# Kernel optimization log

Hardware: AMD Instinct MI355X
Metric: run time of the kernel (lower is better)

Reference implementation:

```python
import jax, jax.numpy as jnp
from jax import lax
import numpy as np

H = 52; W = 52; N = 31; VIS = 256; LANG = 256; HID = 256


def _conv(x, w, b):
    # NCHW conv, SAME padding, stride 1
    return lax.conv_general_dilated(x, w, (1, 1), 'SAME',
                                    dimension_numbers=('NCHW', 'OIHW', 'NCHW')) + b[None, :, None, None]


def setup_inputs() -> dict:
    key = jax.random.key(0)
    ks = jax.random.split(key, 12)

    def kaiming(k, shape):
        fan_in = shape[1] * shape[2] * shape[3]
        return (jax.random.normal(k, shape) * np.sqrt(2.0 / fan_in)).astype(jnp.float32)

    # full binary tree: node c's parent is (c-1)//2; adj[parent, child] = 1; root = 0
    adj = np.zeros((N, N), np.int32)
    for c in range(1, N):
        adj[(c - 1) // 2, c] = 1

    return {
        'vis_feat': jax.random.normal(ks[0], (1, VIS, H, W), jnp.float32),
        'lang_feat': jax.random.normal(ks[1], (N, LANG), jnp.float32),
        'mconv_w': kaiming(ks[2], (HID, 2 * VIS + LANG, 1, 1)), 'mconv_b': jnp.zeros((HID,), jnp.float32),
        'reset_w': kaiming(ks[3], (HID, 2 * HID, 3, 3)), 'reset_b': jnp.zeros((HID,), jnp.float32),
        'update_w': kaiming(ks[4], (HID, 2 * HID, 3, 3)), 'update_b': jnp.zeros((HID,), jnp.float32),
        'output_w': kaiming(ks[5], (HID, 2 * HID, 3, 3)), 'output_b': jnp.zeros((HID,), jnp.float32),
        'theta_v_w': kaiming(ks[6], (128, HID, 1, 1)), 'theta_v_b': jnp.zeros((128,), jnp.float32),
        'theta_l_w': kaiming(ks[7], (128, LANG, 1, 1)), 'theta_l_b': jnp.zeros((128,), jnp.float32),
        'psi_w': kaiming(ks[8], (1, 128, 1, 1)), 'psi_b': jnp.zeros((1,), jnp.float32),
        'W_w': kaiming(ks[9], (HID, HID, 1, 1)), 'W_b': jnp.zeros((HID,), jnp.float32),
        'adj': jnp.asarray(adj),
    }


def reference(vis_feat, lang_feat, mconv_w, mconv_b, reset_w, reset_b, update_w, update_b,
              output_w, output_b, theta_v_w, theta_v_b, theta_l_w, theta_l_b,
              psi_w, psi_b, W_w, W_b, adj):
    adj_np = np.asarray(adj)
    children = [np.nonzero(adj_np[i] > 0)[0] for i in range(adj_np.shape[0])]
    root = int(np.nonzero(adj_np.sum(axis=0) == 0)[0][0])
    hid = reset_w.shape[0]
    Hh, Ww = vis_feat.shape[2], vis_feat.shape[3]

    def gru_cell(x, child_h):
        # x: [1,hid,H,W], child_h: [L,1,hid,H,W]
        L = child_h.shape[0]
        ch_sum = child_h.sum(axis=0)  # [1,hid,H,W]
        z = jax.nn.sigmoid(_conv(jnp.concatenate([x, ch_sum], axis=1), update_w, update_b))
        xr = jnp.broadcast_to(x[None], (L,) + x.shape)
        r_in = jnp.concatenate([xr, child_h], axis=2).reshape(L, 2 * hid, Hh, Ww)
        r = jax.nn.sigmoid(_conv(r_in, reset_w, reset_b))[:, None]  # [L,1,hid,H,W]
        reset_hidden = (r * child_h).sum(axis=0)
        ri = jnp.tanh(_conv(jnp.concatenate([x, reset_hidden], axis=1), output_w, output_b))
        return (1 - z) * ri + z * ch_sum

    def node(idx):
        kids = children[idx]
        if len(kids) == 0:
            child_atts = jnp.zeros((1, 1, Hh, Ww), vis_feat.dtype)
            child_h = jnp.zeros((1, 1, hid, Hh, Ww), vis_feat.dtype)
        else:
            fs, ats = zip(*[node(int(c)) for c in kids])
            child_h = jnp.stack(fs)                  # [L,1,hid,H,W]
            child_atts = jnp.concatenate(ats, 0)     # [L,1,H,W]
        att_in = 1 - child_atts.mean(axis=0, keepdims=True)  # [1,1,H,W]
        ctx = att_in * vis_feat                              # [1,VIS,H,W]
        lang_map = jnp.broadcast_to(lang_feat[idx][None, :, None, None],
                                    (1, lang_feat.shape[1], Hh, Ww))
        nf = _conv(jnp.concatenate([vis_feat, ctx, lang_map], axis=1), mconv_w, mconv_b)
        f = jax.nn.softplus(_conv(nf, theta_v_w, theta_v_b) + _conv(lang_map, theta_l_w, theta_l_b))
        att = jax.nn.sigmoid(_conv(f, psi_w, psi_b))  # [1,1,H,W]
        Wy = _conv(att * nf, W_w, W_b)
        h = gru_cell(Wy, child_h)
        return h, att

    return node(root)
```

## Files before the change

### kernel.cpp

```cpp
#include <hip/hip_runtime.h>
#include <hip/hip_bf16.h>

typedef __hip_bfloat16 bf16;
typedef short bf16x8 __attribute__((ext_vector_type(8)));
typedef float f32x16 __attribute__((ext_vector_type(16)));

static constexpr int  HW2 = 52;
static constexpr int  P2  = 2704;
static constexpr long CHW = 692224L;
static constexpr long PADE  = 884736L;
static constexpr long SLOT_W = 589824L;

static constexpr long O_HPB = 0;
static constexpr long O_XP  = O_HPB + 24*(PADE/2);
static constexpr long O_CS  = O_XP  + 16*(PADE/2);
static constexpr long O_RH  = O_CS  + 8*(PADE/2);
static constexpr long O_Z   = O_RH  + 8*(PADE/2);
static constexpr long O_RX  = O_Z   + 16*(CHW/2);
static constexpr long O_T1  = O_RX  + 8*(CHW/2);
static constexpr long O_T2  = O_T1  + 8*(CHW/2);
static constexpr long O_VPT = O_T2  + 8*(CHW/2);
static constexpr long O_ATT = O_VPT + (long)P2*768;
static constexpr long O_TVL = O_ATT + 31L*P2;
static constexpr long O_WL  = O_TVL + 31L*128;
static constexpr long O_S   = O_WL  + 31L*256;
static constexpr long O_WRE = O_S   + 768L*256;
static constexpr long WS_FLOATS = O_WRE + (3L*2*SLOT_W)/2;
static constexpr long ZERO_F4 = O_Z / 4;

struct ConvDesc {
  const bf16 *in0, *in1;
  const bf16 *w;
  void *out;
  const bf16 *zb;
  const bf16 *h1, *h2;
  long mode;
};
struct ConvBatch { ConvDesc d[32]; };

__device__ __forceinline__ float sigf(float x){ return 1.f/(1.f+expf(-x)); }
__device__ __forceinline__ float softplusf(float x){ return fmaxf(x,0.f) + log1pf(expf(-fabsf(x))); }
__device__ __forceinline__ long padidx(int px, int c){
  int y = px/HW2, x = px - y*HW2;
  return ((long)(c>>4)*3456 + (y+1)*64 + (x+1))*16 + (c&15);
}
__device__ __forceinline__ void gl_lds16(const bf16* g, bf16* l){
  __builtin_amdgcn_global_load_lds((const __attribute__((address_space(1))) void*)g,
                                   (__attribute__((address_space(3))) void*)l, 16, 0, 0);
}

__global__ __launch_bounds__(256) void k_zero(float4* __restrict__ dst, long n4)
{
  long e = (long)blockIdx.x*256 + threadIdx.x;
  if (e < n4) dst[e] = make_float4(0.f,0.f,0.f,0.f);
}

__global__ __launch_bounds__(256) void k_compose(
    const float* __restrict__ theta_v_w, const float* __restrict__ W_w,
    const float* __restrict__ mconv_w, float* __restrict__ S)
{
  int row = blockIdx.x, col = threadIdx.x;
  const float* A; int arow; int bcol;
  if      (row < 128) { A = theta_v_w; arow = row;     bcol = col;       }
  else if (row < 256) { A = theta_v_w; arow = row-128; bcol = col + 256; }
  else if (row < 512) { A = W_w;       arow = row-256; bcol = col;       }
  else                { A = W_w;       arow = row-512; bcol = col + 256; }
  float a = 0.f;
  for (int k=0;k<256;k++) a = fmaf(A[arow*256+k], mconv_w[k*768 + bcol], a);
  S[(long)row*256 + col] = a;
}

__global__ __launch_bounds__(256) void k_nodevec(
    const float* __restrict__ lang, const float* __restrict__ mconv_w, const float* __restrict__ mconv_b,
    const float* __restrict__ theta_v_w, const float* __restrict__ theta_v_b,
    const float* __restrict__ theta_l_w, const float* __restrict__ theta_l_b,
    const float* __restrict__ W_w, float* __restrict__ tvl, float* __restrict__ WLg)
{
  __shared__ float lf[256], lc[256];
  int n = blockIdx.x, tid = threadIdx.x;
  lf[tid] = lang[n*256 + tid];
  __syncthreads();
  float a = mconv_b[tid];
  for (int k=0;k<256;k++) a = fmaf(mconv_w[tid*768 + 512 + k], lf[k], a);
  lc[tid] = a;
  __syncthreads();
  if (tid < 128) {
    float b = theta_v_b[tid] + theta_l_b[tid];
    for (int k=0;k<256;k++) {
      b = fmaf(theta_v_w[tid*256+k], lc[k], b);
      b = fmaf(theta_l_w[tid*256+k], lf[k], b);
    }
    tvl[n*128 + tid] = b;
  }
  float c2 = 0.f;
  for (int k=0;k<256;k++) c2 = fmaf(W_w[tid*256+k], lc[k], c2);
  WLg[n*256 + tid] = c2;
}

__global__ __launch_bounds__(256) void k_vis_gemm(
    const float* __restrict__ S, const float* __restrict__ vis, float* __restrict__ VP)
{
  int p = blockIdx.x*256 + threadIdx.x; if (p >= P2) return;
  int m0 = blockIdx.y*4;
  float a0=0,a1=0,a2=0,a3=0;
  for (int k=0;k<256;k++) {
    float v = vis[k*P2 + p];
    a0 = fmaf(S[(m0+0)*256+k], v, a0);
    a1 = fmaf(S[(m0+1)*256+k], v, a1);
    a2 = fmaf(S[(m0+2)*256+k], v, a2);
    a3 = fmaf(S[(m0+3)*256+k], v, a3);
  }
  VP[(long)(m0+0)*P2+p]=a0; VP[(long)(m0+1)*P2+p]=a1;
  VP[(long)(m0+2)*P2+p]=a2; VP[(long)(m0+3)*P2+p]=a3;
}

__global__ __launch_bounds__(256) void k_vpt(const float* __restrict__ VP, float* __restrict__ VPT)
{
  __shared__ float t[64][65];
  int p0 = blockIdx.x*64, m0 = blockIdx.y*64;
  int c = threadIdx.x & 63, rb = threadIdx.x >> 6;
  for (int r = rb; r < 64; r += 4) {
    int p = p0 + c;
    t[r][c] = (p < P2) ? VP[(long)(m0 + r)*P2 + p] : 0.f;
  }
  __syncthreads();
  for (int r = rb; r < 64; r += 4) {
    int p = p0 + r;
    if (p < P2) VPT[(long)p*768 + (m0 + c)] = t[c][r];
  }
}

__global__ __launch_bounds__(256) void k_wre(
    const float* __restrict__ wu, const float* __restrict__ wr, const float* __restrict__ wo,
    bf16* __restrict__ dst)
{
  long e = (long)blockIdx.x*256 + threadIdx.x;
  int gate = blockIdx.y;
  const float* src = (gate==0) ? wu : (gate==1) ? wr : wo;
  int ci  = e & 15;       long t1 = e >> 4;
  int co  = t1 & 255;     long t2 = t1 >> 8;
  int tap = t2 % 9;       long t3 = t2 / 9;
  int cb  = t3 & 15;      int inp = (int)(t3 >> 4);
  int cin = inp*256 + cb*16 + ci;
  dst[(long)gate*2*SLOT_W + e] = __float2bfloat16(src[((long)co*512 + cin)*9 + tap]);
}

__global__ __launch_bounds__(256) void k_pre(
    const float* __restrict__ VPT, const float* __restrict__ tvl, const float* __restrict__ WLg,
    const float* __restrict__ psi_w, const float* __restrict__ psi_b, const float* __restrict__ W_b,
    float* __restrict__ attp, bf16* __restrict__ xpad, bf16* __restrict__ cspad,
    const bf16* __restrict__ hpb, int n0, int is_leaf)
{
  __shared__ float satt[16], sattin[16];
  const int tid = threadIdx.x, lane = tid & 63, wv = tid >> 6;
  const int i = blockIdx.y, n = n0 + i;
  const int pb = blockIdx.x*16;
  #pragma unroll
  for (int j=0;j<4;j++){
    int sl = wv*4 + j, p = pb + sl;
    float ai = 1.f;
    if (!is_leaf)
      ai = 1.f - 0.5f*(attp[(long)(2*n+1)*P2+p] + attp[(long)(2*n+2)*P2+p]);
    const float* vp = VPT + (long)p*768;
    float t0 = vp[lane]      + ai*vp[128+lane] + tvl[n*128+lane];
    float t1 = vp[64+lane]   + ai*vp[192+lane] + tvl[n*128+64+lane];
    float s = psi_w[lane]*softplusf(t0) + psi_w[64+lane]*softplusf(t1);
    for (int o=32;o;o>>=1) s += __shfl_xor(s,o);
    if (lane==0){
      float av = sigf(s + psi_b[0]);
      satt[sl]=av; sattin[sl]=ai; attp[(long)n*P2+p]=av;
    }
  }
  __syncthreads();
  const int c = tid;
  bf16* xp = xpad + (long)i*PADE;
  bf16* cp = cspad + (long)i*PADE;
  const bf16* h1 = hpb + (long)((2*n+1)%24)*PADE;
  const bf16* h2 = hpb + (long)((2*n+2)%24)*PADE;
  float wl = WLg[n*256+c], wb = W_b[c];
  for (int j=0;j<16;j++){
    int p = pb + j;
    long pi = padidx(p, c);
    const float* vp = VPT + (long)p*768;
    float wy = fmaf(satt[j], vp[256+c] + sattin[j]*vp[512+c] + wl, wb);
    xp[pi] = __float2bfloat16(wy);
    if (!is_leaf)
      cp[pi] = __float2bfloat16(__bfloat162float(h1[pi]) + __bfloat162float(h2[pi]));
  }
}

__global__ __launch_bounds__(256, 4) void k_conv(ConvBatch cb, int Z,
    const float* __restrict__ ub, const float* __restrict__ ob)
{
  __shared__ __align__(16) bf16 simg[8*64*16];
  __shared__ __align__(16) bf16 swt[9*64*16];
  const int L = blockIdx.x + 11*(blockIdx.y + 4*blockIdx.z);
  const int T = 44*Z;
  int V = L;
  if ((T & 7) == 0) V = (L & 7)*(T >> 3) + (L >> 3);
  const int dz  = V / 44;
  const int rr  = V - dz*44;
  const int coh = rr / 11;
  const int pxb = rr - coh*11;
  const ConvDesc d = cb.d[dz];
  const int pxbase = pxb * 256;
  const int co0    = coh * 64;
  const int tid = threadIdx.x, wv = tid >> 6, lane = tid & 63;
  const int wpx = wv * 64;
  const int y0 = pxbase / HW2;
  const int r0 = (y0 > 46) ? 46 : y0;
  const int khalf = lane >> 5;

  int apos[2];
  #pragma unroll
  for (int f=0; f<2; f++) {
    int p = pxbase + wpx + f*32 + (lane & 31);
    if (p >= P2) p = P2-1;
    int y = p / HW2, x = p - y*HW2;
    apos[f] = ((y - r0)*64 + x)*16 + khalf*8;
  }
  const int bpos = (lane & 31)*16 + khalf*8;

  f32x16 acc[2][2];
  #pragma unroll
  for (int f=0;f<2;f++)
    #pragma unroll
    for (int g=0;g<2;g++)
      #pragma unroll
      for (int r=0;r<16;r++) acc[f][g][r] = 0.f;

  const int ninp = d.in1 ? 2 : 1;
  for (int inp = 0; inp < ninp; ++inp) {
    const bf16* __restrict__ in = inp ? d.in1 : d.in0;
    const bf16* __restrict__ wg = d.w + (long)inp * SLOT_W;
    for (int c16 = 0; c16 < 16; ++c16) {
      __syncthreads();
      const long slab = (long)c16*55296 + (long)r0*1024;
      for (int i = wv; i < 34; i += 4) {
        if (i < 16)
          gl_lds16(in + slab + i*512 + lane*8, simg + i*512);
        else {
          int j = i - 16, tap = j >> 1, q = j & 1;
          gl_lds16(wg + (((long)c16*9 + tap)*256 + co0 + q*32)*16 + lane*8,
                   swt + tap*1024 + q*512);
        }
      }
      __syncthreads();
      #pragma unroll
      for (int tap = 0; tap < 9; ++tap) {
        const int toff = ((tap/3)*64 + (tap%3))*16;
        bf16x8 a0 = *(const bf16x8*)(simg + apos[0] + toff);
        bf16x8 a1 = *(const bf16x8*)(simg + apos[1] + toff);
        bf16x8 b0 = *(const bf16x8*)(swt + tap*1024 + bpos);
        bf16x8 b1 = *(const bf16x8*)(swt + tap*1024 + bpos + 512);
        acc[0][0] = __builtin_amdgcn_mfma_f32_32x32x16_bf16(a0, b0, acc[0][0], 0, 0, 0);
        acc[0][1] = __builtin_amdgcn_mfma_f32_32x32x16_bf16(a0, b1, acc[0][1], 0, 0, 0);
        acc[1][0] = __builtin_amdgcn_mfma_f32_32x32x16_bf16(a1, b0, acc[1][0], 0, 0, 0);
        acc[1][1] = __builtin_amdgcn_mfma_f32_32x32x16_bf16(a1, b1, acc[1][1], 0, 0, 0);
      }
    }
  }

  const int m = (int)d.mode;
  #pragma unroll
  for (int f=0;f<2;f++) {
    #pragma unroll
    for (int g=0;g<2;g++) {
      #pragma unroll
      for (int r=0;r<16;r++) {
        int px = pxbase + wpx + f*32 + (r&3) + 8*(r>>2) + 4*khalf;
        if (px >= P2) continue;
        int co = co0 + g*32 + (lane & 31);
        float v = acc[f][g][r];
        if (m == 0) {
          ((bf16*)d.out)[(long)px*256 + co] = __float2bfloat16(v);
        } else if (m == 1) {
          ((bf16*)d.out)[(long)px*256 + co] = __float2bfloat16(sigf(v + ub[co]));
        } else {
          float z = __bfloat162float(d.zb[(long)px*256 + co]);
          long pi = padidx(px, co);
          float cs = 0.f;
          if (d.h1) cs = __bfloat162float(d.h1[pi]) + __bfloat162float(d.h2[pi]);
          ((bf16*)d.out)[pi] = __float2bfloat16((1.f - z)*tanhf(v + ob[co]) + z*cs);
        }
      }
    }
  }
}

__global__ __launch_bounds__(256) void k_fin(
    const bf16* __restrict__ ubuf, const bf16* __restrict__ obuf,
    bf16* __restrict__ hpb, const float* __restrict__ update_b,
    const float* __restrict__ output_b, int n0)
{
  const int c = threadIdx.x, i = blockIdx.y, n = n0 + i;
  const bf16* u = ubuf + (long)i*CHW;
  const bf16* o = obuf + (long)i*CHW;
  bf16* h = hpb + (long)(n%24)*PADE;
  float ubv = update_b[c], obv = output_b[c];
  for (int j=0;j<16;j++){
    int p = blockIdx.x*16 + j;
    long e = (long)p*256 + c;
    float z = sigf(__bfloat162float(u[e]) + ubv);
    h[padidx(p, c)] = __float2bfloat16((1.f - z)*tanhf(__bfloat162float(o[e]) + obv));
  }
}

__global__ __launch_bounds__(256) void k_rh(
    const bf16* __restrict__ rxb, const bf16* __restrict__ t1b, const bf16* __restrict__ t2b,
    bf16* __restrict__ rhpad, const bf16* __restrict__ hpb,
    const float* __restrict__ reset_b, int n0)
{
  const int c = threadIdx.x, i = blockIdx.y, n = n0 + i;
  const bf16* rx = rxb + (long)i*CHW;
  const bf16* t1 = t1b + (long)i*CHW;
  const bf16* t2 = t2b + (long)i*CHW;
  bf16* rh = rhpad + (long)i*PADE;
  const bf16* h1 = hpb + (long)((2*n+1)%24)*PADE;
  const bf16* h2 = hpb + (long)((2*n+2)%24)*PADE;
  float rb = reset_b[c];
  for (int j=0;j<16;j++){
    int p = blockIdx.x*16 + j;
    long e = (long)p*256 + c, pi = padidx(p, c);
    float a = __bfloat162float(rx[e]);
    float r1 = sigf(a + __bfloat162float(t1[e]) + rb);
    float r2 = sigf(a + __bfloat162float(t2[e]) + rb);
    rh[pi] = __float2bfloat16(r1*__bfloat162float(h1[pi]) + r2*__bfloat162float(h2[pi]));
  }
}

__global__ __launch_bounds__(256) void k_outh(const bf16* __restrict__ h0, float* __restrict__ out)
{
  __shared__ float t[64][65];
  int p0 = blockIdx.x*64, c0 = blockIdx.y*64;
  int c = threadIdx.x & 63, rb = threadIdx.x >> 6;
  for (int r = rb; r < 64; r += 4) {
    int p = p0 + r;
    t[r][c] = (p < P2) ? __bfloat162float(h0[padidx(p, c0 + c)]) : 0.f;
  }
  __syncthreads();
  for (int r = rb; r < 64; r += 4) {
    int p = p0 + c;
    if (p < P2) out[(long)(c0 + r)*P2 + p] = t[c][r];
  }
}
__global__ __launch_bounds__(256) void k_outa(const float* __restrict__ att0, float* __restrict__ out)
{
  int p = blockIdx.x*256 + threadIdx.x;
  if (p < P2) out[CHW + p] = att0[p];
}

extern "C" void kernel_launch(void* const* d_in, const int* in_sizes, int n_in,
                              void* d_out, int out_size, void* d_ws, size_t ws_size,
                              hipStream_t stream)
{
  const float* vis       = (const float*)d_in[0];
  const float* lang      = (const float*)d_in[1];
  const float* mconv_w   = (const float*)d_in[2];
  const float* mconv_b   = (const float*)d_in[3];
  const float* reset_w   = (const float*)d_in[4];
  const float* reset_b   = (const float*)d_in[5];
  const float* update_w  = (const float*)d_in[6];
  const float* update_b  = (const float*)d_in[7];
  const float* output_w  = (const float*)d_in[8];
  const float* output_b  = (const float*)d_in[9];
  const float* theta_v_w = (const float*)d_in[10];
  const float* theta_v_b = (const float*)d_in[11];
  const float* theta_l_w = (const float*)d_in[12];
  const float* theta_l_b = (const float*)d_in[13];
  const float* psi_w     = (const float*)d_in[14];
  const float* psi_b     = (const float*)d_in[15];
  const float* W_w       = (const float*)d_in[16];
  const float* W_b       = (const float*)d_in[17];

  if (ws_size < (size_t)WS_FLOATS * sizeof(float)) return;
  float* ws   = (float*)d_ws;
  bf16*  hpb  = (bf16*)(ws + O_HPB);
  bf16*  xpad = (bf16*)(ws + O_XP);
  bf16*  cspad= (bf16*)(ws + O_CS);
  bf16*  rhpad= (bf16*)(ws + O_RH);
  bf16*  zbuf = (bf16*)(ws + O_Z);
  bf16*  rxb  = (bf16*)(ws + O_RX);
  bf16*  t1b  = (bf16*)(ws + O_T1);
  bf16*  t2b  = (bf16*)(ws + O_T2);
  float* VPT  = ws + O_VPT;
  float* attp = ws + O_ATT;
  float* tvl  = ws + O_TVL;
  float* WLg  = ws + O_WL;
  float* S    = ws + O_S;
  bf16*  wre  = (bf16*)(ws + O_WRE);
  bf16*  wre_u = wre;
  bf16*  wre_r = wre + 2*SLOT_W;
  bf16*  wre_o = wre + 4*SLOT_W;
  float* VP   = (float*)zbuf;

  auto hslot = [&](int n){ return hpb + (long)(n%24)*PADE; };
  auto xp    = [&](int i){ return xpad  + (long)i*PADE; };
  auto csp   = [&](int i){ return cspad + (long)i*PADE; };
  auto rhp   = [&](int i){ return rhpad + (long)i*PADE; };
  auto zbp   = [&](int i){ return zbuf + (long)i*CHW; };
  auto obp   = [&](int i){ return rxb + (long)i*CHW; };

  k_zero<<<(ZERO_F4 + 255)/256, 256, 0, stream>>>((float4*)ws, ZERO_F4);
  k_wre<<<dim3(4608,3), 256, 0, stream>>>(update_w, reset_w, output_w, wre);
  k_compose<<<768, 256, 0, stream>>>(theta_v_w, W_w, mconv_w, S);
  k_nodevec<<<31, 256, 0, stream>>>(lang, mconv_w, mconv_b, theta_v_w, theta_v_b,
                                    theta_l_w, theta_l_b, W_w, tvl, WLg);
  k_vis_gemm<<<dim3(11,192), 256, 0, stream>>>(S, vis, VP);
  k_vpt<<<dim3(43,12), 256, 0, stream>>>(VP, VPT);

  {
    const int n0 = 15, B = 16;
    k_pre<<<dim3(169,B), 256, 0, stream>>>(VPT, tvl, WLg, psi_w, psi_b, W_b,
                                           attp, xpad, cspad, hpb, n0, 1);
    ConvBatch ca{};
    for (int i=0;i<B;i++) {
      ca.d[i]   = { xp(i), nullptr, wre_u, (void*)zbp(i), nullptr, nullptr, nullptr, 0 };
      ca.d[B+i] = { xp(i), nullptr, wre_o, (void*)obp(i), nullptr, nullptr, nullptr, 0 };
    }
    k_conv<<<dim3(11,4,2*B), 256, 0, stream>>>(ca, 2*B, update_b, output_b);
    k_fin<<<dim3(169,B), 256, 0, stream>>>(zbuf, rxb, hpb, update_b, output_b, n0);
  }

  const int Ln0[4] = {7, 3, 1, 0};
  const int LnB[4] = {8, 4, 2, 1};
  for (int li=0; li<4; li++) {
    int n0 = Ln0[li]; int B = LnB[li];
    k_pre<<<dim3(169,B), 256, 0, stream>>>(VPT, tvl, WLg, psi_w, psi_b, W_b,
                                           attp, xpad, cspad, hpb, n0, 0);
    ConvBatch ca{};
    for (int i=0;i<B;i++) {
      int n = n0 + i;
      ca.d[4*i+0] = { xp(i), csp(i),    wre_u,          (void*)zbp(i),              nullptr, nullptr, nullptr, 1 };
      ca.d[4*i+1] = { xp(i), nullptr,   wre_r,          (void*)(rxb + (long)i*CHW), nullptr, nullptr, nullptr, 0 };
      ca.d[4*i+2] = { hslot(2*n+1), nullptr, wre_r + SLOT_W, (void*)(t1b + (long)i*CHW), nullptr, nullptr, nullptr, 0 };
      ca.d[4*i+3] = { hslot(2*n+2), nullptr, wre_r + SLOT_W, (void*)(t2b + (long)i*CHW), nullptr, nullptr, nullptr, 0 };
    }
    k_conv<<<dim3(11,4,4*B), 256, 0, stream>>>(ca, 4*B, update_b, output_b);
    k_rh<<<dim3(169,B), 256, 0, stream>>>(rxb, t1b, t2b, rhpad, hpb, reset_b, n0);
    ConvBatch cb2{};
    for (int i=0;i<B;i++) {
      int n = n0 + i;
      cb2.d[i] = { xp(i), rhp(i), wre_o, (void*)hslot(n), zbp(i), hslot(2*n+1), hslot(2*n+2), 2 };
    }
    k_conv<<<dim3(11,4,B), 256, 0, stream>>>(cb2, B, update_b, output_b);
  }

  k_outh<<<dim3(43,4), 256, 0, stream>>>(hslot(0), (float*)d_out);
  k_outa<<<11, 256, 0, stream>>>(attp, (float*)d_out);
}
```

Before: 1.269 ms.

## Split-K conv partials for small upper tree levels to fill the GPU

For the upper tree levels (4, 2 and 1 nodes), the 3x3 conv batches are split along the input-channel dimension into separate descriptors. Each one writes a bf16 partial sum, and the new k_rh2 and k_fin2 kernels add the partials and apply the gate nonlinearities. The aim is more workgroups at levels where the grid is otherwise too small to occupy the device. The cost is extra partial-buffer traffic, bf16 rounding of the partial sums, and one more elementwise kernel per level, since the fused epilogue mode is no longer used there.

```diff
diff --git a/kernel.cpp b/kernel.cpp
--- a/kernel.cpp
+++ b/kernel.cpp
@@ -15,18 +15,15 @@
 static constexpr long O_XP  = O_HPB + 24*(PADE/2);
 static constexpr long O_CS  = O_XP  + 16*(PADE/2);
 static constexpr long O_RH  = O_CS  + 8*(PADE/2);
-static constexpr long O_Z   = O_RH  + 8*(PADE/2);
-static constexpr long O_RX  = O_Z   + 16*(CHW/2);
-static constexpr long O_T1  = O_RX  + 8*(CHW/2);
-static constexpr long O_T2  = O_T1  + 8*(CHW/2);
-static constexpr long O_VPT = O_T2  + 8*(CHW/2);
+static constexpr long O_SL  = O_RH  + 8*(PADE/2);
+static constexpr long O_VPT = O_SL  + 40*(CHW/2);
 static constexpr long O_ATT = O_VPT + (long)P2*768;
 static constexpr long O_TVL = O_ATT + 31L*P2;
 static constexpr long O_WL  = O_TVL + 31L*128;
 static constexpr long O_S   = O_WL  + 31L*256;
 static constexpr long O_WRE = O_S   + 768L*256;
 static constexpr long WS_FLOATS = O_WRE + (3L*2*SLOT_W)/2;
-static constexpr long ZERO_F4 = O_Z / 4;
+static constexpr long ZERO_F4 = O_SL / 4;
 
 struct ConvDesc {
   const bf16 *in0, *in1;
@@ -35,6 +32,7 @@
   const bf16 *zb;
   const bf16 *h1, *h2;
   long mode;
+  int cbeg, cend;
 };
 struct ConvBatch { ConvDesc d[32]; };
 
@@ -233,7 +231,7 @@
   for (int inp = 0; inp < ninp; ++inp) {
     const bf16* __restrict__ in = inp ? d.in1 : d.in0;
     const bf16* __restrict__ wg = d.w + (long)inp * SLOT_W;
-    for (int c16 = 0; c16 < 16; ++c16) {
+    for (int c16 = d.cbeg; c16 < d.cend; ++c16) {
       __syncthreads();
       const long slab = (long)c16*55296 + (long)r0*1024;
       for (int i = wv; i < 34; i += 4) {
@@ -329,6 +327,62 @@
   }
 }
 
+__global__ __launch_bounds__(256) void k_rh2(
+    bf16* __restrict__ uP, const bf16* __restrict__ rxP,
+    const bf16* __restrict__ t1P, const bf16* __restrict__ t2P,
+    bf16* __restrict__ rhpad, const bf16* __restrict__ hpb,
+    const float* __restrict__ update_b, const float* __restrict__ reset_b,
+    int n0, int uS, int rS)
+{
+  const int c = threadIdx.x, i = blockIdx.y, n = n0 + i;
+  bf16* u        = uP  + (long)i*uS*CHW;
+  const bf16* rx = rxP + (long)i*rS*CHW;
+  const bf16* t1 = t1P + (long)i*rS*CHW;
+  const bf16* t2 = t2P + (long)i*rS*CHW;
+  bf16* rh = rhpad + (long)i*PADE;
+  const bf16* h1 = hpb + (long)((2*n+1)%24)*PADE;
+  const bf16* h2 = hpb + (long)((2*n+2)%24)*PADE;
+  float ubv = update_b[c], rb = reset_b[c];
+  for (int j=0;j<16;j++){
+    int p = blockIdx.x*16 + j;
+    long e = (long)p*256 + c, pi = padidx(p, c);
+    float U=0.f, RX=0.f, T1v=0.f, T2v=0.f;
+    for (int s=0;s<uS;s++) U += __bfloat162float(u[(long)s*CHW + e]);
+    for (int s=0;s<rS;s++){
+      RX  += __bfloat162float(rx[(long)s*CHW + e]);
+      T1v += __bfloat162float(t1[(long)s*CHW + e]);
+      T2v += __bfloat162float(t2[(long)s*CHW + e]);
+    }
+    float z  = sigf(U + ubv);
+    float r1 = sigf(RX + T1v + rb), r2 = sigf(RX + T2v + rb);
+    rh[pi] = __float2bfloat16(r1*__bfloat162float(h1[pi]) + r2*__bfloat162float(h2[pi]));
+    u[e] = __float2bfloat16(z);
+  }
+}
+
+__global__ __launch_bounds__(256) void k_fin2(
+    const bf16* __restrict__ oP, const bf16* __restrict__ zP,
+    bf16* __restrict__ hpb, const float* __restrict__ output_b,
+    int n0, int oS, int zstr)
+{
+  const int c = threadIdx.x, i = blockIdx.y, n = n0 + i;
+  const bf16* o  = oP + (long)i*oS*CHW;
+  const bf16* zn = zP + (long)i*zstr*CHW;
+  const bf16* h1 = hpb + (long)((2*n+1)%24)*PADE;
+  const bf16* h2 = hpb + (long)((2*n+2)%24)*PADE;
+  bf16* h = hpb + (long)(n%24)*PADE;
+  float obv = output_b[c];
+  for (int j=0;j<16;j++){
+    int p = blockIdx.x*16 + j;
+    long e = (long)p*256 + c, pi = padidx(p, c);
+    float O=0.f;
+    for (int s=0;s<oS;s++) O += __bfloat162float(o[(long)s*CHW + e]);
+    float z = __bfloat162float(zn[e]);
+    h[pi] = __float2bfloat16((1.f - z)*tanhf(O + obv)
+                             + z*(__bfloat162float(h1[pi]) + __bfloat162float(h2[pi])));
+  }
+}
+
 __global__ __launch_bounds__(256) void k_outh(const bf16* __restrict__ h0, float* __restrict__ out)
 {
   __shared__ float t[64][65];
@@ -379,10 +433,7 @@
   bf16*  xpad = (bf16*)(ws + O_XP);
   bf16*  cspad= (bf16*)(ws + O_CS);
   bf16*  rhpad= (bf16*)(ws + O_RH);
-  bf16*  zbuf = (bf16*)(ws + O_Z);
-  bf16*  rxb  = (bf16*)(ws + O_RX);
-  bf16*  t1b  = (bf16*)(ws + O_T1);
-  bf16*  t2b  = (bf16*)(ws + O_T2);
+  bf16*  slb  = (bf16*)(ws + O_SL);
   float* VPT  = ws + O_VPT;
   float* attp = ws + O_ATT;
   float* tvl  = ws + O_TVL;
@@ -392,14 +443,13 @@
   bf16*  wre_u = wre;
   bf16*  wre_r = wre + 2*SLOT_W;
   bf16*  wre_o = wre + 4*SLOT_W;
-  float* VP   = (float*)zbuf;
+  float* VP   = (float*)slb;
 
   auto hslot = [&](int n){ return hpb + (long)(n%24)*PADE; };
   auto xp    = [&](int i){ return xpad  + (long)i*PADE; };
   auto csp   = [&](int i){ return cspad + (long)i*PADE; };
   auto rhp   = [&](int i){ return rhpad + (long)i*PADE; };
-  auto zbp   = [&](int i){ return zbuf + (long)i*CHW; };
-  auto obp   = [&](int i){ return rxb + (long)i*CHW; };
+  auto slot  = [&](int s){ return slb + (long)s*CHW; };
 
   k_zero<<<(ZERO_F4 + 255)/256, 256, 0, stream>>>((float4*)ws, ZERO_F4);
   k_wre<<<dim3(4608,3), 256, 0, stream>>>(update_w, reset_w, output_w, wre);
@@ -415,35 +465,90 @@
                                            attp, xpad, cspad, hpb, n0, 1);
     ConvBatch ca{};
     for (int i=0;i<B;i++) {
-      ca.d[i]   = { xp(i), nullptr, wre_u, (void*)zbp(i), nullptr, nullptr, nullptr, 0 };
-      ca.d[B+i] = { xp(i), nullptr, wre_o, (void*)obp(i), nullptr, nullptr, nullptr, 0 };
+      ca.d[i]   = { xp(i), nullptr, wre_u, (void*)slot(i),    nullptr, nullptr, nullptr, 0, 0, 16 };
+      ca.d[B+i] = { xp(i), nullptr, wre_o, (void*)slot(16+i), nullptr, nullptr, nullptr, 0, 0, 16 };
     }
     k_conv<<<dim3(11,4,2*B), 256, 0, stream>>>(ca, 2*B, update_b, output_b);
-    k_fin<<<dim3(169,B), 256, 0, stream>>>(zbuf, rxb, hpb, update_b, output_b, n0);
-  }
-
-  const int Ln0[4] = {7, 3, 1, 0};
-  const int LnB[4] = {8, 4, 2, 1};
-  for (int li=0; li<4; li++) {
-    int n0 = Ln0[li]; int B = LnB[li];
+    k_fin<<<dim3(169,B), 256, 0, stream>>>(slot(0), slot(16), hpb, update_b, output_b, n0);
+  }
+
+  {
+    const int n0 = 7, B = 8;
     k_pre<<<dim3(169,B), 256, 0, stream>>>(VPT, tvl, WLg, psi_w, psi_b, W_b,
                                            attp, xpad, cspad, hpb, n0, 0);
     ConvBatch ca{};
     for (int i=0;i<B;i++) {
       int n = n0 + i;
-      ca.d[4*i+0] = { xp(i), csp(i),    wre_u,          (void*)zbp(i),              nullptr, nullptr, nullptr, 1 };
-      ca.d[4*i+1] = { xp(i), nullptr,   wre_r,          (void*)(rxb + (long)i*CHW), nullptr, nullptr, nullptr, 0 };
-      ca.d[4*i+2] = { hslot(2*n+1), nullptr, wre_r + SLOT_W, (void*)(t1b + (long)i*CHW), nullptr, nullptr, nullptr, 0 };
-      ca.d[4*i+3] = { hslot(2*n+2), nullptr, wre_r + SLOT_W, (void*)(t2b + (long)i*CHW), nullptr, nullptr, nullptr, 0 };
+      ca.d[4*i+0] = { xp(i), csp(i),    wre_u,          (void*)slot(i),    nullptr, nullptr, nullptr, 1, 0, 16 };
+      ca.d[4*i+1] = { xp(i), nullptr,   wre_r,          (void*)slot(16+i), nullptr, nullptr, nullptr, 0, 0, 16 };
+      ca.d[4*i+2] = { hslot(2*n+1), nullptr, wre_r + SLOT_W, (void*)slot(24+i), nullptr, nullptr, nullptr, 0, 0, 16 };
+      ca.d[4*i+3] = { hslot(2*n+2), nullptr, wre_r + SLOT_W, (void*)slot(32+i), nullptr, nullptr, nullptr, 0, 0, 16 };
     }
     k_conv<<<dim3(11,4,4*B), 256, 0, stream>>>(ca, 4*B, update_b, output_b);
-    k_rh<<<dim3(169,B), 256, 0, stream>>>(rxb, t1b, t2b, rhpad, hpb, reset_b, n0);
+    k_rh<<<dim3(169,B), 256, 0, stream>>>(slot(16), slot(24), slot(32), rhpad, hpb, reset_b, n0);
     ConvBatch cb2{};
     for (int i=0;i<B;i++) {
       int n = n0 + i;
-      cb2.d[i] = { xp(i), rhp(i), wre_o, (void*)hslot(n), zbp(i), hslot(2*n+1), hslot(2*n+2), 2 };
+      cb2.d[i] = { xp(i), rhp(i), wre_o, (void*)hslot(n), slot(i), hslot(2*n+1), hslot(2*n+2), 2, 0, 16 };
     }
     k_conv<<<dim3(11,4,B), 256, 0, stream>>>(cb2, B, update_b, output_b);
+  }
+
+  const int Tn0[3] = {3, 1, 0};
+  const int TnB[3] = {4, 2, 1};
+  for (int li=0; li<3; li++) {
+    int n0 = Tn0[li]; int B = TnB[li];
+    int uS = (li==0) ? 2 : 4;
+    int rS = (li==0) ? 1 : 2;
+    int oS = (li==0) ? 2 : 4;
+    bf16* uP  = slot(0);
+    bf16* rxP = slot(8);
+    bf16* t1P = slot(8 + B*rS);
+    bf16* t2P = slot(8 + 2*B*rS);
+    bf16* oP  = slot(20);
+    k_pre<<<dim3(169,B), 256, 0, stream>>>(VPT, tvl, WLg, psi_w, psi_b, W_b,
+                                           attp, xpad, cspad, hpb, n0, 0);
+    ConvBatch ca{}; int zi = 0;
+    for (int i=0;i<B;i++) {
+      int n = n0 + i;
+      for (int s=0;s<uS;s++) {
+        const bf16* src; const bf16* w; int c0, c1;
+        if (uS == 2) { src = s ? csp(i) : xp(i); w = s ? wre_u + SLOT_W : wre_u; c0 = 0; c1 = 16; }
+        else { src = (s>>1) ? csp(i) : xp(i); w = (s>>1) ? wre_u + SLOT_W : wre_u; c0 = (s&1)*8; c1 = c0 + 8; }
+        ca.d[zi++] = { src, nullptr, w, (void*)(uP + ((long)i*uS + s)*CHW),
+                       nullptr, nullptr, nullptr, 0, c0, c1 };
+      }
+      for (int s=0;s<rS;s++) {
+        int c0 = (rS==2) ? s*8 : 0, c1 = (rS==2) ? s*8+8 : 16;
+        ca.d[zi++] = { xp(i), nullptr, wre_r, (void*)(rxP + ((long)i*rS + s)*CHW),
+                       nullptr, nullptr, nullptr, 0, c0, c1 };
+      }
+      for (int s=0;s<rS;s++) {
+        int c0 = (rS==2) ? s*8 : 0, c1 = (rS==2) ? s*8+8 : 16;
+        ca.d[zi++] = { hslot(2*n+1), nullptr, wre_r + SLOT_W, (void*)(t1P + ((long)i*rS + s)*CHW),
+                       nullptr, nullptr, nullptr, 0, c0, c1 };
+      }
+      for (int s=0;s<rS;s++) {
+        int c0 = (rS==2) ? s*8 : 0, c1 = (rS==2) ? s*8+8 : 16;
+        ca.d[zi++] = { hslot(2*n+2), nullptr, wre_r + SLOT_W, (void*)(t2P + ((long)i*rS + s)*CHW),
+                       nullptr, nullptr, nullptr, 0, c0, c1 };
+      }
+    }
+    k_conv<<<dim3(11,4,zi), 256, 0, stream>>>(ca, zi, update_b, output_b);
+    k_rh2<<<dim3(169,B), 256, 0, stream>>>(uP, rxP, t1P, t2P, rhpad, hpb,
+                                           update_b, reset_b, n0, uS, rS);
+    ConvBatch cb2{}; int z2 = 0;
+    for (int i=0;i<B;i++) {
+      for (int s=0;s<oS;s++) {
+        const bf16* src; const bf16* w; int c0, c1;
+        if (oS == 2) { src = s ? rhp(i) : xp(i); w = s ? wre_o + SLOT_W : wre_o; c0 = 0; c1 = 16; }
+        else { src = (s>>1) ? rhp(i) : xp(i); w = (s>>1) ? wre_o + SLOT_W : wre_o; c0 = (s&1)*8; c1 = c0 + 8; }
+        cb2.d[z2++] = { src, nullptr, w, (void*)(oP + ((long)i*oS + s)*CHW),
+                        nullptr, nullptr, nullptr, 0, c0, c1 };
+      }
+    }
+    k_conv<<<dim3(11,4,z2), 256, 0, stream>>>(cb2, z2, update_b, output_b);
+    k_fin2<<<dim3(169,B), 256, 0, stream>>>(oP, uP, hpb, output_b, n0, oS, uS);
   }
 
   k_outh<<<dim3(43,4), 256, 0, stream>>>(hslot(0), (float*)d_out);
```

Measured after the change: 1.094 ms. 13.8% less time.
